# Kernel tuning notes

Measured on AMD Instinct MI355X. Metric: run time of the kernel, lower is better.

Reference implementation:

```python
import jax, jax.numpy as jnp
import numpy as np

E = 768      # embed_dim
H = 12       # num_heads
DH = E // H  # head_dim = 64
L = 128      # tgt_len
B = 2        # bsz
NEG_SLOPE = 0.01  # F.leaky_relu default


def setup_inputs() -> dict:
    key = jax.random.key(0)
    ks = jax.random.split(key, 18)
    s = 0.02
    w = lambda k, shape: jax.random.normal(k, shape, dtype=jnp.float32) * s
    return {
        'query': jax.random.normal(ks[0], (L, B, E), dtype=jnp.float32),
        'entity': jax.random.normal(ks[1], (L, B, E), dtype=jnp.float32),
        # Conv1d(E, E, kernel_size=2, padding=1): weight (out, in, 2)
        'conv_w': w(ks[2], (E, E, 2)), 'conv_b': w(ks[3], (E,)),
        # Linear(E, E//2) projections: weight (out, in)
        'q_w': w(ks[4], (E // 2, E)), 'q_b': w(ks[5], (E // 2,)),
        'k_w': w(ks[6], (E // 2, E)), 'k_b': w(ks[7], (E // 2,)),
        'v_w': w(ks[8], (E // 2, E)), 'v_b': w(ks[9], (E // 2,)),
        'e_w': w(ks[10], (E // 2, E)), 'e_b': w(ks[11], (E // 2,)),
        # attn_fc: Linear(3*head_dim, 1)
        'attn_w': w(ks[12], (1, 3 * DH)), 'attn_b': w(ks[13], (1,)),
        # ConvTranspose1d(E, E, kernel_size=2): weight (in, out, 2)
        'deconv_w': w(ks[14], (E, E, 2)), 'deconv_b': w(ks[15], (E,)),
        'out_w': w(ks[16], (E, E)), 'out_b': w(ks[17], (E,)),
    }


def _prev(x):
    # x shifted by one along time (zero-padded at t=0): x_prev[t] = x[t-1]
    return jnp.concatenate([jnp.zeros_like(x[:1]), x[:-1]], axis=0)


def _forward(query, entity, conv_w, conv_b, q_w, q_b, k_w, k_b, v_w, v_b,
             e_w, e_b, attn_w, attn_b, deconv_w, deconv_b, out_w, out_b):
    Lq, Bq, _ = query.shape
    BH = Bq * H
    lin = lambda x, W, b: x @ W.T + b

    # conv1D(query) with padding=1, then slice [:, :, :L]:
    # out[t] = W[:,:,0] @ x[t-1] + W[:,:,1] @ x[t] + b   (x[-1] = 0)
    nq = (jnp.einsum('oi,lbi->lbo', conv_w[:, :, 0], _prev(query)) +
          jnp.einsum('oi,lbi->lbo', conv_w[:, :, 1], query) + conv_b)

    e = lin(entity, e_w, e_b)           # (L, B, E/2)
    q = lin(nq, q_w, q_b)
    k = lin(nq, k_w, k_b)               # self-attention: k, v from conv'd query
    v = lin(nq, v_w, v_b)

    # _shape: view(L, B*H, Dh).transpose(0, 1) -> (B*H, L, Dh)
    shp = lambda t: t.reshape(Lq, BH, DH).transpose(1, 0, 2)
    qe = shp(jnp.concatenate([q, e], axis=-1))
    ke = shp(jnp.concatenate([k, e], axis=-1))
    ve = shp(jnp.concatenate([v, e], axis=-1))

    # edge[i, j, b] = entity[i, b] - entity[j, b]; then raw row-major view
    # (L, L, B, E) -> (B*H, L, L, Dh), exactly matching torch .contiguous().view
    edge = (entity[:, None] - entity[None, :]).reshape(BH, Lq, Lq, DH)

    # qe: transpose(0,1).repeat(L,1,1,1).transpose(0,1).reshape(BH, L, L, Dh)
    # yields T[x, y, m, d] = qe[m, x, d], then raw row-major reshape
    qe_big = jnp.broadcast_to(qe.transpose(1, 0, 2)[:, None],
                              (Lq, Lq, BH, DH)).reshape(BH, Lq, Lq, DH)
    # ke: repeat(L,1,1,1).reshape -> R[a, m, l, d] = ke[m, l, d], raw reshape
    ke_big = jnp.broadcast_to(ke[None], (Lq, BH, Lq, DH)).reshape(BH, Lq, Lq, DH)

    # attn_fc(cat([qe, ke, edge], -1)).squeeze() as three partial dots
    wv = attn_w[0]
    scores = (jnp.einsum('bijd,d->bij', qe_big, wv[:DH]) +
              jnp.einsum('bijd,d->bij', ke_big, wv[DH:2 * DH]) +
              jnp.einsum('bijd,d->bij', edge, wv[2 * DH:]) + attn_b[0])
    scores = jnp.where(scores >= 0, scores, NEG_SLOPE * scores)  # leaky_relu

    probs = jax.nn.softmax(scores, axis=-1)  # dropout p=0 -> no-op
    attn = jnp.einsum('bij,bjd->bid', probs, ve)          # (B*H, L, Dh)
    a = attn.transpose(1, 0, 2).reshape(Lq, Bq, E)        # (L, B, E)

    # deconv1D (ConvTranspose1d k=2), slice [:, :, :L]:
    # out[t] = W[:,:,0]^T x[t] + W[:,:,1]^T x[t-1] + b
    y = (jnp.einsum('io,lbi->lbo', deconv_w[:, :, 0], a) +
         jnp.einsum('io,lbi->lbo', deconv_w[:, :, 1], _prev(a)) + deconv_b)

    return lin(y, out_w, out_b)


def reference(query, entity, conv_w, conv_b, q_w, q_b, k_w, k_b, v_w, v_b,
              e_w, e_b, attn_w, attn_b, deconv_w, deconv_b, out_w, out_b):
    return _forward(query, entity, conv_w, conv_b, q_w, q_b, k_w, k_b,
                    v_w, v_b, e_w, e_b, attn_w, attn_b, deconv_w, deconv_b,
                    out_w, out_b)
```

## Files before the change

kernel.cpp:

```cpp
#include <hip/hip_runtime.h>
#include <hip/hip_bf16.h>

#define LQ 128
#define BZ 2
#define EE 768
#define EH 384
#define NH 12
#define DHD 64
#define BHD 24
#define MM 256

__device__ inline float wsum(float v) {
#pragma unroll
  for (int off = 32; off; off >>= 1) v += __shfl_xor(v, off, 64);
  return v;
}

template <int TAPMODE>
__device__ __forceinline__ void conv_core(const float* __restrict__ A,
                                          const float* __restrict__ W,
                                          float* __restrict__ C,
                                          int m0, int n0, int kbase, float* smem) {
  float* As  = smem;
  float* Bs0 = smem + 1152;
  float* Bs1 = Bs0 + 2176;
  const int tid = threadIdx.x;
  const int ar = tid >> 3, ak4 = (tid & 7) << 2;
  const int gmA = m0 - 2 + ar;
  const bool extra = (tid < 16);
  const int ar2 = 32 + (tid >> 3);
  const int gmA2 = m0 + 30 + (tid >> 3);
  const int tn = tid & 15, tm = tid >> 4;

  const int bn = tid >> 2, ig = tid & 3;
  const int il = tid >> 3, ng = tid & 7;

  float4 pa, pa2, pb[4];
  auto ld = [&](int kt) {
    int gi = kbase + kt;
    pa = (gmA >= 0) ? *(const float4*)(A + (size_t)gmA * 768 + gi + ak4)
                    : make_float4(0.f, 0.f, 0.f, 0.f);
    if (extra) pa2 = *(const float4*)(A + (size_t)gmA2 * 768 + gi + ak4);
    if (TAPMODE == 0) {
      const float* wrow = W + (size_t)(n0 + bn) * 1536 + 2 * (gi + ig * 8);
#pragma unroll
      for (int c = 0; c < 4; ++c) pb[c] = *(const float4*)(wrow + 4 * c);
    } else {
      const float* wrow = W + (size_t)(gi + il) * 1536 + 2 * (n0 + ng * 8);
#pragma unroll
      for (int c = 0; c < 4; ++c) pb[c] = *(const float4*)(wrow + 4 * c);
    }
  };

  ld(0);
  float acc[2][4] = {};
  for (int kt = 0; kt < 384; kt += 32) {
#pragma unroll
    for (int c = 0; c < 4; ++c) {
      float v = (c == 0) ? pa.x : (c == 1) ? pa.y : (c == 2) ? pa.z : pa.w;
      As[(ak4 + c) * 36 + ar] = v;
    }
    if (extra) {
#pragma unroll
      for (int c = 0; c < 4; ++c) {
        float v = (c == 0) ? pa2.x : (c == 1) ? pa2.y : (c == 2) ? pa2.z : pa2.w;
        As[(ak4 + c) * 36 + ar2] = v;
      }
    }
    if (TAPMODE == 0) {
#pragma unroll
      for (int c = 0; c < 4; ++c) {
        int i_l = ig * 8 + 2 * c;
        Bs0[i_l * 68 + bn] = pb[c].x; Bs1[i_l * 68 + bn] = pb[c].y;
        Bs0[(i_l + 1) * 68 + bn] = pb[c].z; Bs1[(i_l + 1) * 68 + bn] = pb[c].w;
      }
    } else {
#pragma unroll
      for (int c = 0; c < 4; ++c) {
        int n_l = ng * 8 + 2 * c;
        Bs0[il * 68 + n_l] = pb[c].x; Bs1[il * 68 + n_l] = pb[c].y;
        Bs0[il * 68 + n_l + 1] = pb[c].z; Bs1[il * 68 + n_l + 1] = pb[c].w;
      }
    }
    __syncthreads();
    if (kt + 32 < 384) ld(kt + 32);
#pragma unroll
    for (int i = 0; i < 32; ++i) {
      float4 b0 = *(const float4*)(Bs0 + i * 68 + (tn << 2));
      float4 b1 = *(const float4*)(Bs1 + i * 68 + (tn << 2));
      float ap0 = As[i * 36 + (tm << 1)];
      float ap1 = As[i * 36 + (tm << 1) + 1];
      float ac0 = As[i * 36 + (tm << 1) + 2];
      float ac1 = As[i * 36 + (tm << 1) + 3];
      float bc[4] = {b0.x, b0.y, b0.z, b0.w};
      float bp[4] = {b1.x, b1.y, b1.z, b1.w};
#pragma unroll
      for (int jj = 0; jj < 4; ++jj) {
        if (TAPMODE == 0) {
          acc[0][jj] += ac0 * bp[jj] + ap0 * bc[jj];
          acc[1][jj] += ac1 * bp[jj] + ap1 * bc[jj];
        } else {
          acc[0][jj] += ac0 * bc[jj] + ap0 * bp[jj];
          acc[1][jj] += ac1 * bc[jj] + ap1 * bp[jj];
        }
      }
    }
    __syncthreads();
  }
#pragma unroll
  for (int j = 0; j < 2; ++j) {
    int m = m0 + (tm << 1) + j;
    float4 o = make_float4(acc[j][0], acc[j][1], acc[j][2], acc[j][3]);
    *(float4*)(C + (size_t)m * 768 + n0 + (tn << 2)) = o;
  }
}

template <bool SUM2, bool ATOMIC>
__device__ __forceinline__ void gemm_plain(const float* __restrict__ A,
                                           const float* __restrict__ A2,
                                           const float* __restrict__ ab,
                                           const float* __restrict__ Bw,
                                           const float* __restrict__ bias,
                                           float* __restrict__ C, int N,
                                           int m0, int n0, int kbase, int kchunk,
                                           float* smem) {
  float* As = smem;
  float* Bs = smem + 1152;
  const int tid = threadIdx.x;
  const int ar = tid >> 3, ak4 = (tid & 7) << 2;
  const int br = tid >> 2, bk4 = (tid & 3) << 2;
  const int tn = tid & 15, tm = tid >> 4;
  const float* Arow = A + (size_t)(m0 + ar) * 768;
  const float* A2row = A2 ? A2 + (size_t)(m0 + ar) * 768 : nullptr;
  const float* Brow = Bw + (size_t)(n0 + br) * 768;
  float4 pa, pb0, pb1;
  auto ld = [&](int kt) {
    int gi = kbase + kt;
    pa = *(const float4*)(Arow + gi + ak4);
    if (SUM2) {
      float4 t2 = *(const float4*)(A2row + gi + ak4);
      float4 t3 = *(const float4*)(ab + gi + ak4);
      pa.x += t2.x + t3.x; pa.y += t2.y + t3.y;
      pa.z += t2.z + t3.z; pa.w += t2.w + t3.w;
    }
    pb0 = *(const float4*)(Brow + gi + bk4);
    pb1 = *(const float4*)(Brow + gi + bk4 + 16);
  };
  ld(0);
  float acc[2][4] = {};
  for (int kt = 0; kt < kchunk; kt += 32) {
    As[(ak4 + 0) * 36 + ar] = pa.x; As[(ak4 + 1) * 36 + ar] = pa.y;
    As[(ak4 + 2) * 36 + ar] = pa.z; As[(ak4 + 3) * 36 + ar] = pa.w;
    Bs[(bk4 + 0) * 68 + br] = pb0.x; Bs[(bk4 + 1) * 68 + br] = pb0.y;
    Bs[(bk4 + 2) * 68 + br] = pb0.z; Bs[(bk4 + 3) * 68 + br] = pb0.w;
    Bs[(bk4 + 16) * 68 + br] = pb1.x; Bs[(bk4 + 17) * 68 + br] = pb1.y;
    Bs[(bk4 + 18) * 68 + br] = pb1.z; Bs[(bk4 + 19) * 68 + br] = pb1.w;
    __syncthreads();
    if (kt + 32 < kchunk) ld(kt + 32);
#pragma unroll
    for (int k = 0; k < 32; ++k) {
      float2 a2 = *(const float2*)(As + k * 36 + (tm << 1));
      float4 b4 = *(const float4*)(Bs + k * 68 + (tn << 2));
      float aa[2] = {a2.x, a2.y};
      float bb[4] = {b4.x, b4.y, b4.z, b4.w};
#pragma unroll
      for (int i = 0; i < 2; ++i)
#pragma unroll
        for (int j = 0; j < 4; ++j) acc[i][j] += aa[i] * bb[j];
    }
    __syncthreads();
  }
#pragma unroll
  for (int i = 0; i < 2; ++i) {
    int m = m0 + (tm << 1) + i;
#pragma unroll
    for (int j = 0; j < 4; ++j) {
      int n = n0 + (tn << 2) + j;
      if (ATOMIC) {
        float bv = bias ? bias[n] : 0.f;
        unsafeAtomicAdd(&C[(size_t)m * N + n], acc[i][j] + bv);
      } else {
        C[(size_t)m * N + n] = acc[i][j] + bias[n];
      }
    }
  }
}

__global__ __launch_bounds__(256) void k1_fused(
    const float* __restrict__ query, const float* __restrict__ entity,
    const float* __restrict__ conv_w, const float* __restrict__ e_w,
    const float* __restrict__ e_b, const float* __restrict__ q_w,
    const float* __restrict__ q_b, const float* __restrict__ k_w,
    const float* __restrict__ k_b, const float* __restrict__ wv,
    float* __restrict__ nq0, float* __restrict__ nq1, float* __restrict__ e_buf,
    float* __restrict__ qw_red, float* __restrict__ kw_red,
    float* __restrict__ qb_red, float* __restrict__ kb_red,
    float* __restrict__ Ewbuf) {
  __shared__ float smem[5504];
  int bid = blockIdx.x;
  if (bid < 192) {
    int kz = bid / 96, t = bid % 96;
    int m0 = (t / 12) * 32, n0 = (t % 12) * 64;
    conv_core<0>(query, conv_w, kz ? nq1 : nq0, m0, n0, kz * 384, smem);
  } else if (bid < 240) {
    int t = bid - 192;
    int m0 = (t / 6) * 32, n0 = (t % 6) * 64;
    gemm_plain<false, false>(entity, nullptr, nullptr, e_w, e_b, e_buf, 384,
                             m0, n0, 0, 768, smem);
  } else if (bid < 279) {
    int W = (bid - 240) * 4 + (threadIdx.x >> 6);
    int lane = threadIdx.x & 63;
    if (W < 72) {
      int h = W / 12, ib = W % 12, i = ib * 64 + lane;
      float s = 0.f;
#pragma unroll 8
      for (int d = 0; d < 64; ++d) s += q_w[(h * 64 + d) * 768 + i] * wv[d];
      qw_red[h * 768 + i] = s;
    } else if (W < 144) {
      int r = W - 72;
      int h = r / 12, ib = r % 12, i = ib * 64 + lane;
      float s = 0.f;
#pragma unroll 8
      for (int d = 0; d < 64; ++d) s += k_w[(h * 64 + d) * 768 + i] * wv[64 + d];
      kw_red[h * 768 + i] = s;
    } else if (W < 156) {
      int r = W - 144;
      float s;
      if (r < 6) {
        s = wsum(q_b[r * 64 + lane] * wv[lane]);
        if (lane == 0) qb_red[r] = s;
      } else {
        s = wsum(k_b[(r - 6) * 64 + lane] * wv[64 + lane]);
        if (lane == 0) kb_red[r - 6] = s;
      }
    }
  } else {
    int row = (bid - 279) * 4 + (threadIdx.x >> 6);
    int lane = threadIdx.x & 63;
    const float* erow = entity + (size_t)row * 768;
    float wvl = wv[128 + lane];
#pragma unroll
    for (int cb = 0; cb < 12; ++cb) {
      float s = wsum(erow[cb * 64 + lane] * wvl);
      if (lane == 0) Ewbuf[row * 12 + cb] = s;
    }
  }
}

__global__ __launch_bounds__(256) void k2_fused(
    const float* __restrict__ nq0, const float* __restrict__ nq1,
    const float* __restrict__ conv_b, const float* __restrict__ v_w,
    const float* __restrict__ v_b, const float* __restrict__ e_buf,
    const float* __restrict__ qw_red, const float* __restrict__ kw_red,
    const float* __restrict__ qb_red, const float* __restrict__ kb_red,
    const float* __restrict__ wv, float* __restrict__ v_buf,
    float* __restrict__ Abuf, float* __restrict__ Bkbuf) {
  __shared__ float smem[3328];
  int bid = blockIdx.x;
  if (bid < 48) {
    int m0 = (bid / 6) * 32, n0 = (bid % 6) * 64;
    gemm_plain<true, false>(nq0, nq1, conv_b, v_w, v_b, v_buf, 384,
                            m0, n0, 0, 768, smem);
    return;
  }
  int W = (bid - 48) * 4 + (threadIdx.x >> 6);
  int lane = threadIdx.x & 63;
  if (W < 1536) {
    int x = W & 127, q = W >> 7;
    int b = q / 6, h = q % 6;
    const size_t row = (size_t)(x * 2 + b) * 768;
    const float* ww = qw_red + h * 768;
    float p = 0.f;
#pragma unroll
    for (int it = 0; it < 12; ++it) {
      int i = it * 64 + lane;
      p += (nq0[row + i] + nq1[row + i] + conv_b[i]) * ww[i];
    }
    float s = wsum(p) + qb_red[h];
    if (lane == 0) Abuf[(b * 12 + h) * 128 + x] = s;
  } else if (W < 3072) {
    int r = W - 1536;
    int x = r & 127, q = r >> 7;
    int b = q / 6, he = q % 6;
    float s = wsum(e_buf[(size_t)(x * 2 + b) * 384 + he * 64 + lane] * wv[lane]);
    if (lane == 0) Abuf[(b * 12 + 6 + he) * 128 + x] = s;
  } else if (W < 4608) {
    int r = W - 3072;
    int l = r & 127, q = r >> 7;
    int b = q / 6, h = q % 6;
    const size_t row = (size_t)(l * 2 + b) * 768;
    const float* ww = kw_red + h * 768;
    float p = 0.f;
#pragma unroll
    for (int it = 0; it < 12; ++it) {
      int i = it * 64 + lane;
      p += (nq0[row + i] + nq1[row + i] + conv_b[i]) * ww[i];
    }
    float s = wsum(p) + kb_red[h];
    if (lane == 0) Bkbuf[(b * 12 + h) * 128 + l] = s;
  } else {
    int r = W - 4608;
    int l = r & 127, q = r >> 7;
    int b = q / 6, he = q % 6;
    float s = wsum(e_buf[(size_t)(l * 2 + b) * 384 + he * 64 + lane] * wv[64 + lane]);
    if (lane == 0) Bkbuf[(b * 12 + 6 + he) * 128 + l] = s;
  }
}

__global__ __launch_bounds__(128) void attn_kernel(
    const float* __restrict__ Abuf, const float* __restrict__ Bkbuf,
    const float* __restrict__ Ewbuf, const float* __restrict__ attn_b,
    const float* __restrict__ v_buf, const float* __restrict__ e_buf,
    float* __restrict__ a_out) {
  int bh = blockIdx.x >> 7, i2 = blockIdx.x & 127;
  int tid = threadIdx.x;
  int j = tid;
  int G = bh * 16384 + i2 * 128 + j;
  int mq = G % 24, xq = (G / 24) >> 7;
  int mk = (bh * 128 + i2) % 24;
  int cb = G % 12, gb = G / 12;
  int be = gb & 1, ij = gb >> 1, ie = ij >> 7, je = ij & 127;
  float s = Abuf[mq * 128 + xq] + Bkbuf[mk * 128 + j] + Ewbuf[ie * 24 + be * 12 + cb] -
            Ewbuf[je * 24 + be * 12 + cb] + attn_b[0];
  s = s >= 0.f ? s : 0.01f * s;

  __shared__ float ps[128];
  __shared__ float red[4];
  int lane = tid & 63, wid = tid >> 6;
  float mv = s;
#pragma unroll
  for (int off = 32; off; off >>= 1) mv = fmaxf(mv, __shfl_xor(mv, off, 64));
  if (lane == 0) red[wid] = mv;
  __syncthreads();
  float gmax = fmaxf(red[0], red[1]);
  float ex = expf(s - gmax);
  float sv = wsum(ex);
  if (lane == 0) red[2 + wid] = sv;
  __syncthreads();
  float gsum = red[2] + red[3];
  ps[tid] = ex / gsum;
  __syncthreads();

  int d = tid & 63, half = tid >> 6;
  int b = bh / 12, h = bh % 12;
  const float* src = (h < 6) ? (v_buf + h * 64) : (e_buf + (h - 6) * 64);
  float acc = 0.f;
#pragma unroll 4
  for (int jj = 0; jj < 64; ++jj) {
    int jx = half * 64 + jj;
    acc += ps[jx] * src[(size_t)(jx * 2 + b) * 384 + d];
  }
  __shared__ float pv[2][64];
  pv[half][d] = acc;
  __syncthreads();
  if (tid < 64) {
    a_out[(size_t)(i2 * 2 + b) * 768 + h * 64 + tid] = pv[0][tid] + pv[1][tid];
  }
}

__global__ __launch_bounds__(256) void k4_deconv(const float* __restrict__ a_buf,
                                                 const float* __restrict__ deconv_w,
                                                 float* __restrict__ y0,
                                                 float* __restrict__ y1) {
  __shared__ float smem[5504];
  int bid = blockIdx.x;
  int kz = bid / 96, t = bid % 96;
  int m0 = (t / 12) * 32, n0 = (t % 12) * 64;
  conv_core<1>(a_buf, deconv_w, kz ? y1 : y0, m0, n0, kz * 384, smem);
}

__global__ __launch_bounds__(256) void k5_out(const float* __restrict__ y0,
                                              const float* __restrict__ y1,
                                              const float* __restrict__ deconv_b,
                                              const float* __restrict__ out_w,
                                              const float* __restrict__ out_b,
                                              float* __restrict__ dout) {
  __shared__ float smem[3328];
  int bid = blockIdx.x;
  int kz = bid / 96, t = bid % 96;
  int m0 = (t / 12) * 32, n0 = (t % 12) * 64;
  gemm_plain<true, true>(y0, y1, deconv_b, out_w, kz == 0 ? out_b : nullptr,
                         dout, 768, m0, n0, kz * 384, 384, smem);
}

extern "C" void kernel_launch(void* const* d_in, const int* in_sizes, int n_in,
                              void* d_out, int out_size, void* d_ws, size_t ws_size,
                              hipStream_t stream) {
  const float* query    = (const float*)d_in[0];
  const float* entity   = (const float*)d_in[1];
  const float* conv_w   = (const float*)d_in[2];
  const float* conv_b   = (const float*)d_in[3];
  const float* q_w      = (const float*)d_in[4];
  const float* q_b      = (const float*)d_in[5];
  const float* k_w      = (const float*)d_in[6];
  const float* k_b      = (const float*)d_in[7];
  const float* v_w      = (const float*)d_in[8];
  const float* v_b      = (const float*)d_in[9];
  const float* e_w      = (const float*)d_in[10];
  const float* e_b      = (const float*)d_in[11];
  const float* attn_w   = (const float*)d_in[12];
  const float* attn_b   = (const float*)d_in[13];
  const float* deconv_w = (const float*)d_in[14];
  const float* deconv_b = (const float*)d_in[15];
  const float* out_w    = (const float*)d_in[16];
  const float* out_b    = (const float*)d_in[17];

  float* ws     = (float*)d_ws;
  float* nq0    = ws;
  float* nq1    = nq0 + 196608;
  float* e_buf  = nq1 + 196608;
  float* v_buf  = e_buf + 98304;
  float* qw_red = v_buf + 98304;
  float* kw_red = qw_red + 4608;
  float* qb_red = kw_red + 4608;
  float* kb_red = qb_red + 8;
  float* Abuf   = kb_red + 8;
  float* Bkbuf  = Abuf + 3072;
  float* Ewbuf  = Bkbuf + 3072;
  float* a_buf  = Ewbuf + 3072;
  float* y0     = a_buf + 196608;
  float* y1     = y0 + 196608;

  float* dout = (float*)d_out;

  k1_fused<<<343, 256, 0, stream>>>(query, entity, conv_w, e_w, e_b, q_w, q_b,
                                    k_w, k_b, attn_w, nq0, nq1, e_buf, qw_red,
                                    kw_red, qb_red, kb_red, Ewbuf);
  k2_fused<<<1584, 256, 0, stream>>>(nq0, nq1, conv_b, v_w, v_b, e_buf, qw_red,
                                     kw_red, qb_red, kb_red, attn_w, v_buf,
                                     Abuf, Bkbuf);
  attn_kernel<<<3072, 128, 0, stream>>>(Abuf, Bkbuf, Ewbuf, attn_b, v_buf,
                                        e_buf, a_buf);
  k4_deconv<<<192, 256, 0, stream>>>(a_buf, deconv_w, y0, y1);
  k5_out<<<192, 256, 0, stream>>>(y0, y1, deconv_b, out_w, out_b, dout);
}
```

Measured before the change: 209.5 us.

## Merge five kernels into one cooperative persistent kernel with grid syncs

Replaces the five separate launches with a single cooperative kernel of 256 blocks that runs each stage in turn, separated by grid-wide syncs. The conv stage drops its split-K halves and computes the full reduction with the bias folded in, so later stages read a single nq buffer. The output GEMM drops its atomic split-K. Attention work is strided across the persistent blocks, two rows per block at a time. This removes launch gaps and atomics but gives up parallelism: fewer blocks run the GEMMs over a longer K loop, and the attention stage loses the wide launch it had before.

```diff
diff --git a/kernel.cpp b/kernel.cpp
--- a/kernel.cpp
+++ b/kernel.cpp
@@ -1,14 +1,7 @@
 #include <hip/hip_runtime.h>
-#include <hip/hip_bf16.h>
-
-#define LQ 128
-#define BZ 2
-#define EE 768
-#define EH 384
-#define NH 12
-#define DHD 64
-#define BHD 24
-#define MM 256
+#include <hip/hip_cooperative_groups.h>
+
+namespace cg = cooperative_groups;
 
 __device__ inline float wsum(float v) {
 #pragma unroll
@@ -16,11 +9,21 @@
   return v;
 }
 
+struct MegaParams {
+  const float *query, *entity, *conv_w, *conv_b, *q_w, *q_b, *k_w, *k_b;
+  const float *v_w, *v_b, *e_w, *e_b, *attn_w, *attn_b, *deconv_w, *deconv_b;
+  const float *out_w, *out_b;
+  float *nq, *e_buf, *v_buf, *qw_red, *kw_red, *qb_red, *kb_red;
+  float *Abuf, *Bkbuf, *Ewbuf, *a_buf, *y0, *y1, *dout;
+};
+
 template <int TAPMODE>
 __device__ __forceinline__ void conv_core(const float* __restrict__ A,
                                           const float* __restrict__ W,
+                                          const float* __restrict__ bias,
                                           float* __restrict__ C,
-                                          int m0, int n0, int kbase, float* smem) {
+                                          int m0, int n0, int kbase, int kcount,
+                                          float* smem) {
   float* As  = smem;
   float* Bs0 = smem + 1152;
   float* Bs1 = Bs0 + 2176;
@@ -31,7 +34,6 @@
   const int ar2 = 32 + (tid >> 3);
   const int gmA2 = m0 + 30 + (tid >> 3);
   const int tn = tid & 15, tm = tid >> 4;
-
   const int bn = tid >> 2, ig = tid & 3;
   const int il = tid >> 3, ng = tid & 7;
 
@@ -54,7 +56,7 @@
 
   ld(0);
   float acc[2][4] = {};
-  for (int kt = 0; kt < 384; kt += 32) {
+  for (int kt = 0; kt < kcount; kt += 32) {
 #pragma unroll
     for (int c = 0; c < 4; ++c) {
       float v = (c == 0) ? pa.x : (c == 1) ? pa.y : (c == 2) ? pa.z : pa.w;
@@ -83,7 +85,7 @@
       }
     }
     __syncthreads();
-    if (kt + 32 < 384) ld(kt + 32);
+    if (kt + 32 < kcount) ld(kt + 32);
 #pragma unroll
     for (int i = 0; i < 32; ++i) {
       float4 b0 = *(const float4*)(Bs0 + i * 68 + (tn << 2));
@@ -110,20 +112,24 @@
 #pragma unroll
   for (int j = 0; j < 2; ++j) {
     int m = m0 + (tm << 1) + j;
-    float4 o = make_float4(acc[j][0], acc[j][1], acc[j][2], acc[j][3]);
+    float b0 = bias ? bias[n0 + (tn << 2) + 0] : 0.f;
+    float b1 = bias ? bias[n0 + (tn << 2) + 1] : 0.f;
+    float b2 = bias ? bias[n0 + (tn << 2) + 2] : 0.f;
+    float b3 = bias ? bias[n0 + (tn << 2) + 3] : 0.f;
+    float4 o = make_float4(acc[j][0] + b0, acc[j][1] + b1,
+                           acc[j][2] + b2, acc[j][3] + b3);
     *(float4*)(C + (size_t)m * 768 + n0 + (tn << 2)) = o;
   }
 }
 
-template <bool SUM2, bool ATOMIC>
+template <bool SUM2>
 __device__ __forceinline__ void gemm_plain(const float* __restrict__ A,
                                            const float* __restrict__ A2,
                                            const float* __restrict__ ab,
                                            const float* __restrict__ Bw,
                                            const float* __restrict__ bias,
                                            float* __restrict__ C, int N,
-                                           int m0, int n0, int kbase, int kchunk,
-                                           float* smem) {
+                                           int m0, int n0, float* smem) {
   float* As = smem;
   float* Bs = smem + 1152;
   const int tid = threadIdx.x;
@@ -131,11 +137,10 @@
   const int br = tid >> 2, bk4 = (tid & 3) << 2;
   const int tn = tid & 15, tm = tid >> 4;
   const float* Arow = A + (size_t)(m0 + ar) * 768;
-  const float* A2row = A2 ? A2 + (size_t)(m0 + ar) * 768 : nullptr;
+  const float* A2row = SUM2 ? A2 + (size_t)(m0 + ar) * 768 : nullptr;
   const float* Brow = Bw + (size_t)(n0 + br) * 768;
   float4 pa, pb0, pb1;
-  auto ld = [&](int kt) {
-    int gi = kbase + kt;
+  auto ld = [&](int gi) {
     pa = *(const float4*)(Arow + gi + ak4);
     if (SUM2) {
       float4 t2 = *(const float4*)(A2row + gi + ak4);
@@ -148,7 +153,7 @@
   };
   ld(0);
   float acc[2][4] = {};
-  for (int kt = 0; kt < kchunk; kt += 32) {
+  for (int kt = 0; kt < 768; kt += 32) {
     As[(ak4 + 0) * 36 + ar] = pa.x; As[(ak4 + 1) * 36 + ar] = pa.y;
     As[(ak4 + 2) * 36 + ar] = pa.z; As[(ak4 + 3) * 36 + ar] = pa.w;
     Bs[(bk4 + 0) * 68 + br] = pb0.x; Bs[(bk4 + 1) * 68 + br] = pb0.y;
@@ -156,7 +161,7 @@
     Bs[(bk4 + 16) * 68 + br] = pb1.x; Bs[(bk4 + 17) * 68 + br] = pb1.y;
     Bs[(bk4 + 18) * 68 + br] = pb1.z; Bs[(bk4 + 19) * 68 + br] = pb1.w;
     __syncthreads();
-    if (kt + 32 < kchunk) ld(kt + 32);
+    if (kt + 32 < 768) ld(kt + 32);
 #pragma unroll
     for (int k = 0; k < 32; ++k) {
       float2 a2 = *(const float2*)(As + k * 36 + (tm << 1));
@@ -173,264 +178,223 @@
 #pragma unroll
   for (int i = 0; i < 2; ++i) {
     int m = m0 + (tm << 1) + i;
-#pragma unroll
-    for (int j = 0; j < 4; ++j) {
-      int n = n0 + (tn << 2) + j;
-      if (ATOMIC) {
-        float bv = bias ? bias[n] : 0.f;
-        unsafeAtomicAdd(&C[(size_t)m * N + n], acc[i][j] + bv);
-      } else {
-        C[(size_t)m * N + n] = acc[i][j] + bias[n];
-      }
-    }
+    const float* bp = bias + n0 + (tn << 2);
+    float4 o = make_float4(acc[i][0] + bp[0], acc[i][1] + bp[1],
+                           acc[i][2] + bp[2], acc[i][3] + bp[3]);
+    *(float4*)(C + (size_t)m * N + n0 + (tn << 2)) = o;
   }
 }
 
-__global__ __launch_bounds__(256) void k1_fused(
-    const float* __restrict__ query, const float* __restrict__ entity,
-    const float* __restrict__ conv_w, const float* __restrict__ e_w,
-    const float* __restrict__ e_b, const float* __restrict__ q_w,
-    const float* __restrict__ q_b, const float* __restrict__ k_w,
-    const float* __restrict__ k_b, const float* __restrict__ wv,
-    float* __restrict__ nq0, float* __restrict__ nq1, float* __restrict__ e_buf,
-    float* __restrict__ qw_red, float* __restrict__ kw_red,
-    float* __restrict__ qb_red, float* __restrict__ kb_red,
-    float* __restrict__ Ewbuf) {
+__global__ __launch_bounds__(256) void mega_kernel(MegaParams p) {
+  cg::grid_group grid = cg::this_grid();
   __shared__ float smem[5504];
-  int bid = blockIdx.x;
-  if (bid < 192) {
-    int kz = bid / 96, t = bid % 96;
-    int m0 = (t / 12) * 32, n0 = (t % 12) * 64;
-    conv_core<0>(query, conv_w, kz ? nq1 : nq0, m0, n0, kz * 384, smem);
-  } else if (bid < 240) {
-    int t = bid - 192;
-    int m0 = (t / 6) * 32, n0 = (t % 6) * 64;
-    gemm_plain<false, false>(entity, nullptr, nullptr, e_w, e_b, e_buf, 384,
-                             m0, n0, 0, 768, smem);
-  } else if (bid < 279) {
-    int W = (bid - 240) * 4 + (threadIdx.x >> 6);
-    int lane = threadIdx.x & 63;
+  const int bid = blockIdx.x;
+  const int tid = threadIdx.x;
+  const int wv4 = tid >> 6, lane = tid & 63;
+
+  if (bid < 96) {
+    conv_core<0>(p.query, p.conv_w, p.conv_b, p.nq,
+                 (bid / 12) * 32, (bid % 12) * 64, 0, 768, smem);
+  } else if (bid < 144) {
+    int t = bid - 96;
+    gemm_plain<false>(p.entity, nullptr, nullptr, p.e_w, p.e_b, p.e_buf, 384,
+                      (t / 6) * 32, (t % 6) * 64, smem);
+  } else if (bid < 183) {
+    int W = (bid - 144) * 4 + wv4;
     if (W < 72) {
       int h = W / 12, ib = W % 12, i = ib * 64 + lane;
       float s = 0.f;
 #pragma unroll 8
-      for (int d = 0; d < 64; ++d) s += q_w[(h * 64 + d) * 768 + i] * wv[d];
-      qw_red[h * 768 + i] = s;
+      for (int d = 0; d < 64; ++d) s += p.q_w[(h * 64 + d) * 768 + i] * p.attn_w[d];
+      p.qw_red[h * 768 + i] = s;
     } else if (W < 144) {
       int r = W - 72;
       int h = r / 12, ib = r % 12, i = ib * 64 + lane;
       float s = 0.f;
 #pragma unroll 8
-      for (int d = 0; d < 64; ++d) s += k_w[(h * 64 + d) * 768 + i] * wv[64 + d];
-      kw_red[h * 768 + i] = s;
+      for (int d = 0; d < 64; ++d) s += p.k_w[(h * 64 + d) * 768 + i] * p.attn_w[64 + d];
+      p.kw_red[h * 768 + i] = s;
     } else if (W < 156) {
       int r = W - 144;
-      float s;
       if (r < 6) {
-        s = wsum(q_b[r * 64 + lane] * wv[lane]);
-        if (lane == 0) qb_red[r] = s;
+        float s = wsum(p.q_b[r * 64 + lane] * p.attn_w[lane]);
+        if (lane == 0) p.qb_red[r] = s;
       } else {
-        s = wsum(k_b[(r - 6) * 64 + lane] * wv[64 + lane]);
-        if (lane == 0) kb_red[r - 6] = s;
-      }
-    }
-  } else {
-    int row = (bid - 279) * 4 + (threadIdx.x >> 6);
-    int lane = threadIdx.x & 63;
-    const float* erow = entity + (size_t)row * 768;
-    float wvl = wv[128 + lane];
+        float s = wsum(p.k_b[(r - 6) * 64 + lane] * p.attn_w[64 + lane]);
+        if (lane == 0) p.kb_red[r - 6] = s;
+      }
+    }
+  } else if (bid < 247) {
+    int row = (bid - 183) * 4 + wv4;
+    const float* erow = p.entity + (size_t)row * 768;
+    float wvl = p.attn_w[128 + lane];
 #pragma unroll
     for (int cb = 0; cb < 12; ++cb) {
       float s = wsum(erow[cb * 64 + lane] * wvl);
-      if (lane == 0) Ewbuf[row * 12 + cb] = s;
-    }
-  }
-}
-
-__global__ __launch_bounds__(256) void k2_fused(
-    const float* __restrict__ nq0, const float* __restrict__ nq1,
-    const float* __restrict__ conv_b, const float* __restrict__ v_w,
-    const float* __restrict__ v_b, const float* __restrict__ e_buf,
-    const float* __restrict__ qw_red, const float* __restrict__ kw_red,
-    const float* __restrict__ qb_red, const float* __restrict__ kb_red,
-    const float* __restrict__ wv, float* __restrict__ v_buf,
-    float* __restrict__ Abuf, float* __restrict__ Bkbuf) {
-  __shared__ float smem[3328];
-  int bid = blockIdx.x;
+      if (lane == 0) p.Ewbuf[row * 12 + cb] = s;
+    }
+  }
+  grid.sync();
+
   if (bid < 48) {
-    int m0 = (bid / 6) * 32, n0 = (bid % 6) * 64;
-    gemm_plain<true, false>(nq0, nq1, conv_b, v_w, v_b, v_buf, 384,
-                            m0, n0, 0, 768, smem);
-    return;
-  }
-  int W = (bid - 48) * 4 + (threadIdx.x >> 6);
-  int lane = threadIdx.x & 63;
-  if (W < 1536) {
-    int x = W & 127, q = W >> 7;
-    int b = q / 6, h = q % 6;
-    const size_t row = (size_t)(x * 2 + b) * 768;
-    const float* ww = qw_red + h * 768;
-    float p = 0.f;
-#pragma unroll
-    for (int it = 0; it < 12; ++it) {
-      int i = it * 64 + lane;
-      p += (nq0[row + i] + nq1[row + i] + conv_b[i]) * ww[i];
-    }
-    float s = wsum(p) + qb_red[h];
-    if (lane == 0) Abuf[(b * 12 + h) * 128 + x] = s;
-  } else if (W < 3072) {
-    int r = W - 1536;
-    int x = r & 127, q = r >> 7;
-    int b = q / 6, he = q % 6;
-    float s = wsum(e_buf[(size_t)(x * 2 + b) * 384 + he * 64 + lane] * wv[lane]);
-    if (lane == 0) Abuf[(b * 12 + 6 + he) * 128 + x] = s;
-  } else if (W < 4608) {
-    int r = W - 3072;
-    int l = r & 127, q = r >> 7;
-    int b = q / 6, h = q % 6;
-    const size_t row = (size_t)(l * 2 + b) * 768;
-    const float* ww = kw_red + h * 768;
-    float p = 0.f;
-#pragma unroll
-    for (int it = 0; it < 12; ++it) {
-      int i = it * 64 + lane;
-      p += (nq0[row + i] + nq1[row + i] + conv_b[i]) * ww[i];
-    }
-    float s = wsum(p) + kb_red[h];
-    if (lane == 0) Bkbuf[(b * 12 + h) * 128 + l] = s;
+    gemm_plain<false>(p.nq, nullptr, nullptr, p.v_w, p.v_b, p.v_buf, 384,
+                      (bid / 6) * 32, (bid % 6) * 64, smem);
   } else {
-    int r = W - 4608;
-    int l = r & 127, q = r >> 7;
-    int b = q / 6, he = q % 6;
-    float s = wsum(e_buf[(size_t)(l * 2 + b) * 384 + he * 64 + lane] * wv[64 + lane]);
-    if (lane == 0) Bkbuf[(b * 12 + 6 + he) * 128 + l] = s;
-  }
-}
-
-__global__ __launch_bounds__(128) void attn_kernel(
-    const float* __restrict__ Abuf, const float* __restrict__ Bkbuf,
-    const float* __restrict__ Ewbuf, const float* __restrict__ attn_b,
-    const float* __restrict__ v_buf, const float* __restrict__ e_buf,
-    float* __restrict__ a_out) {
-  int bh = blockIdx.x >> 7, i2 = blockIdx.x & 127;
-  int tid = threadIdx.x;
-  int j = tid;
-  int G = bh * 16384 + i2 * 128 + j;
-  int mq = G % 24, xq = (G / 24) >> 7;
-  int mk = (bh * 128 + i2) % 24;
-  int cb = G % 12, gb = G / 12;
-  int be = gb & 1, ij = gb >> 1, ie = ij >> 7, je = ij & 127;
-  float s = Abuf[mq * 128 + xq] + Bkbuf[mk * 128 + j] + Ewbuf[ie * 24 + be * 12 + cb] -
-            Ewbuf[je * 24 + be * 12 + cb] + attn_b[0];
-  s = s >= 0.f ? s : 0.01f * s;
-
-  __shared__ float ps[128];
-  __shared__ float red[4];
-  int lane = tid & 63, wid = tid >> 6;
-  float mv = s;
-#pragma unroll
-  for (int off = 32; off; off >>= 1) mv = fmaxf(mv, __shfl_xor(mv, off, 64));
-  if (lane == 0) red[wid] = mv;
-  __syncthreads();
-  float gmax = fmaxf(red[0], red[1]);
-  float ex = expf(s - gmax);
-  float sv = wsum(ex);
-  if (lane == 0) red[2 + wid] = sv;
-  __syncthreads();
-  float gsum = red[2] + red[3];
-  ps[tid] = ex / gsum;
-  __syncthreads();
-
-  int d = tid & 63, half = tid >> 6;
-  int b = bh / 12, h = bh % 12;
-  const float* src = (h < 6) ? (v_buf + h * 64) : (e_buf + (h - 6) * 64);
-  float acc = 0.f;
-#pragma unroll 4
-  for (int jj = 0; jj < 64; ++jj) {
-    int jx = half * 64 + jj;
-    acc += ps[jx] * src[(size_t)(jx * 2 + b) * 384 + d];
-  }
-  __shared__ float pv[2][64];
-  pv[half][d] = acc;
-  __syncthreads();
-  if (tid < 64) {
-    a_out[(size_t)(i2 * 2 + b) * 768 + h * 64 + tid] = pv[0][tid] + pv[1][tid];
-  }
-}
-
-__global__ __launch_bounds__(256) void k4_deconv(const float* __restrict__ a_buf,
-                                                 const float* __restrict__ deconv_w,
-                                                 float* __restrict__ y0,
-                                                 float* __restrict__ y1) {
-  __shared__ float smem[5504];
-  int bid = blockIdx.x;
-  int kz = bid / 96, t = bid % 96;
-  int m0 = (t / 12) * 32, n0 = (t % 12) * 64;
-  conv_core<1>(a_buf, deconv_w, kz ? y1 : y0, m0, n0, kz * 384, smem);
-}
-
-__global__ __launch_bounds__(256) void k5_out(const float* __restrict__ y0,
-                                              const float* __restrict__ y1,
-                                              const float* __restrict__ deconv_b,
-                                              const float* __restrict__ out_w,
-                                              const float* __restrict__ out_b,
-                                              float* __restrict__ dout) {
-  __shared__ float smem[3328];
-  int bid = blockIdx.x;
-  int kz = bid / 96, t = bid % 96;
-  int m0 = (t / 12) * 32, n0 = (t % 12) * 64;
-  gemm_plain<true, true>(y0, y1, deconv_b, out_w, kz == 0 ? out_b : nullptr,
-                         dout, 768, m0, n0, kz * 384, 384, smem);
+    int wid = (bid - 48) * 4 + wv4;
+    for (int W = wid; W < 6144; W += 832) {
+      if (W < 1536) {
+        int x = W & 127, q = W >> 7;
+        int b = q / 6, h = q % 6;
+        const size_t row = (size_t)(x * 2 + b) * 768;
+        const float* ww = p.qw_red + h * 768;
+        float pacc = 0.f;
+#pragma unroll
+        for (int it = 0; it < 12; ++it) {
+          int i = it * 64 + lane;
+          pacc += p.nq[row + i] * ww[i];
+        }
+        float s = wsum(pacc) + p.qb_red[h];
+        if (lane == 0) p.Abuf[(b * 12 + h) * 128 + x] = s;
+      } else if (W < 3072) {
+        int r = W - 1536;
+        int x = r & 127, q = r >> 7;
+        int b = q / 6, he = q % 6;
+        float s = wsum(p.e_buf[(size_t)(x * 2 + b) * 384 + he * 64 + lane] * p.attn_w[lane]);
+        if (lane == 0) p.Abuf[(b * 12 + 6 + he) * 128 + x] = s;
+      } else if (W < 4608) {
+        int r = W - 3072;
+        int l = r & 127, q = r >> 7;
+        int b = q / 6, h = q % 6;
+        const size_t row = (size_t)(l * 2 + b) * 768;
+        const float* ww = p.kw_red + h * 768;
+        float pacc = 0.f;
+#pragma unroll
+        for (int it = 0; it < 12; ++it) {
+          int i = it * 64 + lane;
+          pacc += p.nq[row + i] * ww[i];
+        }
+        float s = wsum(pacc) + p.kb_red[h];
+        if (lane == 0) p.Bkbuf[(b * 12 + h) * 128 + l] = s;
+      } else {
+        int r = W - 4608;
+        int l = r & 127, q = r >> 7;
+        int b = q / 6, he = q % 6;
+        float s = wsum(p.e_buf[(size_t)(l * 2 + b) * 384 + he * 64 + lane] * p.attn_w[64 + lane]);
+        if (lane == 0) p.Bkbuf[(b * 12 + 6 + he) * 128 + l] = s;
+      }
+    }
+  }
+  grid.sync();
+
+  {
+    float* ps   = smem;
+    float* redm = smem + 256;
+    float* reds = smem + 260;
+    float* pv   = smem + 264;
+    const int half = tid >> 7;
+    const int t = tid & 127;
+    const int widx = (tid >> 6) & 1;
+    const float ab0 = p.attn_b[0];
+    for (int r = 0; r < 6; ++r) {
+      int u = bid * 12 + 2 * r + half;
+      int bh = u >> 7, i2 = u & 127;
+      int j = t;
+      int G = u * 128 + j;
+      int mq = G % 24, xq = (G / 24) >> 7;
+      int mk = u % 24;
+      int cb = G % 12, gb = G / 12;
+      int be = gb & 1, ij = gb >> 1, ie = ij >> 7, je = ij & 127;
+      float s = p.Abuf[mq * 128 + xq] + p.Bkbuf[mk * 128 + j] +
+                p.Ewbuf[ie * 24 + be * 12 + cb] - p.Ewbuf[je * 24 + be * 12 + cb] + ab0;
+      s = s >= 0.f ? s : 0.01f * s;
+
+      float mv = s;
+#pragma unroll
+      for (int off = 32; off; off >>= 1) mv = fmaxf(mv, __shfl_xor(mv, off, 64));
+      if (lane == 0) redm[half * 2 + widx] = mv;
+      __syncthreads();
+      float gmax = fmaxf(redm[half * 2], redm[half * 2 + 1]);
+      float ex = expf(s - gmax);
+      float sv = wsum(ex);
+      if (lane == 0) reds[half * 2 + widx] = sv;
+      __syncthreads();
+      float gsum = reds[half * 2] + reds[half * 2 + 1];
+      ps[half * 128 + t] = ex / gsum;
+      __syncthreads();
+
+      int d = t & 63, jh = t >> 6;
+      int b = bh / 12, h = bh % 12;
+      const float* src = (h < 6) ? (p.v_buf + h * 64) : (p.e_buf + (h - 6) * 64);
+      float acc = 0.f;
+#pragma unroll 8
+      for (int jj = 0; jj < 64; ++jj) {
+        int jx = jh * 64 + jj;
+        acc += ps[half * 128 + jx] * src[(size_t)(jx * 2 + b) * 384 + d];
+      }
+      pv[half * 128 + jh * 64 + d] = acc;
+      __syncthreads();
+      if (t < 64) {
+        p.a_buf[(size_t)(i2 * 2 + b) * 768 + h * 64 + t] =
+            pv[half * 128 + t] + pv[half * 128 + 64 + t];
+      }
+      __syncthreads();
+    }
+  }
+  grid.sync();
+
+  if (bid < 192) {
+    int kz = bid / 96, t = bid % 96;
+    conv_core<1>(p.a_buf, p.deconv_w, nullptr, kz ? p.y1 : p.y0,
+                 (t / 12) * 32, (t % 12) * 64, kz * 384, 384, smem);
+  }
+  grid.sync();
+
+  if (bid < 96) {
+    gemm_plain<true>(p.y0, p.y1, p.deconv_b, p.out_w, p.out_b, p.dout, 768,
+                     (bid / 12) * 32, (bid % 12) * 64, smem);
+  }
 }
 
 extern "C" void kernel_launch(void* const* d_in, const int* in_sizes, int n_in,
                               void* d_out, int out_size, void* d_ws, size_t ws_size,
                               hipStream_t stream) {
-  const float* query    = (const float*)d_in[0];
-  const float* entity   = (const float*)d_in[1];
-  const float* conv_w   = (const float*)d_in[2];
-  const float* conv_b   = (const float*)d_in[3];
-  const float* q_w      = (const float*)d_in[4];
-  const float* q_b      = (const float*)d_in[5];
-  const float* k_w      = (const float*)d_in[6];
-  const float* k_b      = (const float*)d_in[7];
-  const float* v_w      = (const float*)d_in[8];
-  const float* v_b      = (const float*)d_in[9];
-  const float* e_w      = (const float*)d_in[10];
-  const float* e_b      = (const float*)d_in[11];
-  const float* attn_w   = (const float*)d_in[12];
-  const float* attn_b   = (const float*)d_in[13];
-  const float* deconv_w = (const float*)d_in[14];
-  const float* deconv_b = (const float*)d_in[15];
-  const float* out_w    = (const float*)d_in[16];
-  const float* out_b    = (const float*)d_in[17];
-
-  float* ws     = (float*)d_ws;
-  float* nq0    = ws;
-  float* nq1    = nq0 + 196608;
-  float* e_buf  = nq1 + 196608;
-  float* v_buf  = e_buf + 98304;
-  float* qw_red = v_buf + 98304;
-  float* kw_red = qw_red + 4608;
-  float* qb_red = kw_red + 4608;
-  float* kb_red = qb_red + 8;
-  float* Abuf   = kb_red + 8;
-  float* Bkbuf  = Abuf + 3072;
-  float* Ewbuf  = Bkbuf + 3072;
-  float* a_buf  = Ewbuf + 3072;
-  float* y0     = a_buf + 196608;
-  float* y1     = y0 + 196608;
-
-  float* dout = (float*)d_out;
-
-  k1_fused<<<343, 256, 0, stream>>>(query, entity, conv_w, e_w, e_b, q_w, q_b,
-                                    k_w, k_b, attn_w, nq0, nq1, e_buf, qw_red,
-                                    kw_red, qb_red, kb_red, Ewbuf);
-  k2_fused<<<1584, 256, 0, stream>>>(nq0, nq1, conv_b, v_w, v_b, e_buf, qw_red,
-                                     kw_red, qb_red, kb_red, attn_w, v_buf,
-                                     Abuf, Bkbuf);
-  attn_kernel<<<3072, 128, 0, stream>>>(Abuf, Bkbuf, Ewbuf, attn_b, v_buf,
-                                        e_buf, a_buf);
-  k4_deconv<<<192, 256, 0, stream>>>(a_buf, deconv_w, y0, y1);
-  k5_out<<<192, 256, 0, stream>>>(y0, y1, deconv_b, out_w, out_b, dout);
+  MegaParams p;
+  p.query    = (const float*)d_in[0];
+  p.entity   = (const float*)d_in[1];
+  p.conv_w   = (const float*)d_in[2];
+  p.conv_b   = (const float*)d_in[3];
+  p.q_w      = (const float*)d_in[4];
+  p.q_b      = (const float*)d_in[5];
+  p.k_w      = (const float*)d_in[6];
+  p.k_b      = (const float*)d_in[7];
+  p.v_w      = (const float*)d_in[8];
+  p.v_b      = (const float*)d_in[9];
+  p.e_w      = (const float*)d_in[10];
+  p.e_b      = (const float*)d_in[11];
+  p.attn_w   = (const float*)d_in[12];
+  p.attn_b   = (const float*)d_in[13];
+  p.deconv_w = (const float*)d_in[14];
+  p.deconv_b = (const float*)d_in[15];
+  p.out_w    = (const float*)d_in[16];
+  p.out_b    = (const float*)d_in[17];
+
+  float* ws  = (float*)d_ws;
+  p.nq     = ws;
+  p.e_buf  = p.nq + 196608;
+  p.v_buf  = p.e_buf + 98304;
+  p.qw_red = p.v_buf + 98304;
+  p.kw_red = p.qw_red + 4608;
+  p.qb_red = p.kw_red + 4608;
+  p.kb_red = p.qb_red + 8;
+  p.Abuf   = p.kb_red + 8;
+  p.Bkbuf  = p.Abuf + 3072;
+  p.Ewbuf  = p.Bkbuf + 3072;
+  p.a_buf  = p.Ewbuf + 3072;
+  p.y0     = p.a_buf + 196608;
+  p.y1     = p.y0 + 196608;
+  p.dout   = (float*)d_out;
+
+  void* args[] = {&p};
+  hipLaunchCooperativeKernel((const void*)mega_kernel, dim3(256), dim3(256),
+                             args, 0, stream);
 }
```

Measured after the change: 373.3 us. +78.1%, slower.
